# Optimization experiments

Hardware: AMD Instinct MI355X
Metric: run time of the kernel (lower is better)

## Reference

```python
import jax, jax.numpy as jnp
import numpy as np
import math

D_MODEL, D_STATE, D_CONV, EXPAND = 1024, 16, 4, 2
D_INNER = EXPAND * D_MODEL
DT_RANK = math.ceil(D_MODEL / 16)
BATCH, SEQLEN = 2, 2048


def setup_inputs() -> dict:
    key = jax.random.key(0)
    ks = jax.random.split(key, 10)
    hidden_states = jax.random.normal(ks[0], (BATCH, SEQLEN, D_MODEL), dtype=jnp.float32)
    in_proj_w = jax.random.normal(ks[1], (2 * D_INNER, D_MODEL), dtype=jnp.float32) / math.sqrt(D_MODEL)
    conv_w = jax.random.normal(ks[2], (D_INNER, 1, D_CONV), dtype=jnp.float32) / math.sqrt(D_CONV)
    conv_b = jnp.zeros((D_INNER,), dtype=jnp.float32)
    x_proj_w = jax.random.normal(ks[3], (DT_RANK + 2 * D_STATE, D_INNER), dtype=jnp.float32) / math.sqrt(D_INNER)
    dt_init_std = DT_RANK ** (-0.5)
    dt_proj_w = jax.random.uniform(ks[4], (D_INNER, DT_RANK), dtype=jnp.float32, minval=-dt_init_std, maxval=dt_init_std)
    # dt bias: inverse softplus of dt ~ LogUniform(1e-3, 1e-1), as in the original init
    dt = jnp.exp(jax.random.uniform(ks[5], (D_INNER,), dtype=jnp.float32) * (math.log(0.1) - math.log(0.001)) + math.log(0.001))
    dt = jnp.clip(dt, 1e-4, None)
    dt_proj_b = dt + jnp.log(-jnp.expm1(-dt))
    # A = -exp(A_log), A_log = log(1..d_state) broadcast over d_inner
    A_log = jnp.log(jnp.tile(jnp.arange(1, D_STATE + 1, dtype=jnp.float32)[None, :], (D_INNER, 1)))
    D = jnp.ones((D_INNER,), dtype=jnp.float32)
    out_proj_w = jax.random.normal(ks[6], (D_MODEL, D_INNER), dtype=jnp.float32) / math.sqrt(D_INNER)
    return {
        'hidden_states': hidden_states, 'in_proj_w': in_proj_w, 'conv_w': conv_w,
        'conv_b': conv_b, 'x_proj_w': x_proj_w, 'dt_proj_w': dt_proj_w,
        'dt_proj_b': dt_proj_b, 'A_log': A_log, 'D': D, 'out_proj_w': out_proj_w,
    }


def reference(hidden_states, in_proj_w, conv_w, conv_b, x_proj_w, dt_proj_w, dt_proj_b, A_log, D, out_proj_w):
    B_, L, _ = hidden_states.shape
    d_inner, d_state = A_log.shape
    K = conv_w.shape[-1]
    dt_rank = x_proj_w.shape[0] - 2 * d_state

    # in_proj: (b,l,d_model) -> (b,l,2*d_inner); split into x, z
    xz = hidden_states @ in_proj_w.T
    x, z = jnp.split(xz, 2, axis=-1)

    # causal depthwise conv1d (padding=K-1, truncated to seqlen) + SiLU
    w = conv_w[:, 0, :]  # (d_inner, K)
    xp = jnp.pad(x, ((0, 0), (K - 1, 0), (0, 0)))
    x = sum(xp[:, k:k + L, :] * w[:, k] for k in range(K)) + conv_b
    x = jax.nn.silu(x)

    # x_proj -> dt, B, C
    x_dbl = x @ x_proj_w.T  # (b,l,dt_rank+2n)
    dt, Bm, Cm = jnp.split(x_dbl, [dt_rank, dt_rank + d_state], axis=-1)
    delta = jax.nn.softplus(dt @ dt_proj_w.T + dt_proj_b)  # (b,l,d_inner)
    A = -jnp.exp(A_log)  # (d_inner, d_state)

    # selective scan over time
    def step(h, inp):
        d_t, B_t, C_t, u_t = inp  # (b,d),(b,n),(b,n),(b,d)
        dA = jnp.exp(d_t[:, :, None] * A)                      # (b,d,n)
        h = h * dA + (d_t * u_t)[:, :, None] * B_t[:, None, :]  # (b,d,n)
        y = jnp.einsum('bdn,bn->bd', h, C_t)
        return h, y

    h0 = jnp.zeros((B_, d_inner, d_state), dtype=hidden_states.dtype)
    xs = (jnp.swapaxes(delta, 0, 1), jnp.swapaxes(Bm, 0, 1),
          jnp.swapaxes(Cm, 0, 1), jnp.swapaxes(x, 0, 1))
    _, ys = jax.lax.scan(step, h0, xs)  # ys: (l,b,d_inner)
    y = jnp.swapaxes(ys, 0, 1) + D * x
    y = y * jax.nn.silu(z)
    return y @ out_proj_w.T  # (b,l,d_model)
```

## Files before the change

### kernel.cpp

```cpp
#include <hip/hip_runtime.h>
#include <hip/hip_bf16.h>
#include <math.h>
#include <stddef.h>

#define BATCH   2
#define SEQLEN  2048
#define DMODEL  1024
#define DINNER  2048
#define DSTATE  16
#define DCONV   4
#define DTRANK  64
#define NROWS   (BATCH*SEQLEN)
#define LCH     32
#define NCH     (SEQLEN/LCH)
#define MB      1048576

using ab_frag = __attribute__((ext_vector_type(8))) short;
using cd_frag = __attribute__((ext_vector_type(4))) float;

__device__ __forceinline__ unsigned short f2bf(float f) {
    unsigned u = __float_as_uint(f);
    u = (u + 0x7FFFu + ((u >> 16) & 1u)) >> 16;
    return (unsigned short)u;
}
__device__ __forceinline__ float bf2f(unsigned short h) {
    return __uint_as_float(((unsigned)h) << 16);
}

__device__ __forceinline__ void gll16(const unsigned short* g, unsigned short* l) {
    __builtin_amdgcn_global_load_lds(
        (const __attribute__((address_space(1))) void*)g,
        (__attribute__((address_space(3))) void*)l, 16, 0, 0);
}

__device__ __forceinline__ void pow_chain(float q, float* e) {
    float q2 = q * q;
    float q4 = q2 * q2;
    float q8 = q4 * q4;
    e[0] = q;       e[1] = q2;      e[2] = q2 * q;  e[3] = q4;
    e[4] = q4 * q;  e[5] = q4 * q2; e[6] = q4 * q2 * q; e[7] = q8;
    e[8] = q8 * q;  e[9] = q8 * q2; e[10] = q8 * q2 * q; e[11] = q8 * q4;
    e[12] = q8 * q4 * q; e[13] = q8 * q4 * q2; e[14] = q8 * q4 * q2 * q;
    e[15] = q8 * q8;
}

__global__ void cvt_multi(
    const float* __restrict__ s0, unsigned short* __restrict__ d0, int n0,
    const float* __restrict__ s1, unsigned short* __restrict__ d1, int n1,
    const float* __restrict__ s2, unsigned short* __restrict__ d2, int n2,
    const float* __restrict__ s3, unsigned short* __restrict__ d3, int n3,
    const float* __restrict__ s4, unsigned short* __restrict__ d4, int n4)
{
    int i = blockIdx.x * 256 + threadIdx.x;
    const float* s; unsigned short* d;
    if (i < n0)              { s = s0; d = d0; }
    else if ((i -= n0) < n1) { s = s1; d = d1; }
    else if ((i -= n1) < n2) { s = s2; d = d2; }
    else if ((i -= n2) < n3) { s = s3; d = d3; }
    else if ((i -= n3) < n4) { s = s4; d = d4; }
    else return;
    float4 v = ((const float4*)s)[i];
    ushort4 o;
    o.x = f2bf(v.x); o.y = f2bf(v.y); o.z = f2bf(v.z); o.w = f2bf(v.w);
    ((ushort4*)d)[i] = o;
}

__global__ void reduce2(const float* __restrict__ p, float* __restrict__ out, int n4) {
    int i = blockIdx.x * 256 + threadIdx.x;
    if (i < n4) {
        float4 a = ((const float4*)p)[i];
        float4 b = ((const float4*)p)[i + 1048576];
        float4 o; o.x = a.x + b.x; o.y = a.y + b.y; o.z = a.z + b.z; o.w = a.w + b.w;
        ((float4*)out)[i] = o;
    }
}

__global__ void reduce8_cvt(const float* __restrict__ p,
                            float* __restrict__ xdbl,
                            unsigned short* __restrict__ xdblbf, int n4) {
    int i = blockIdx.x * 256 + threadIdx.x;
    if (i < n4) {
        float4 a = ((const float4*)p)[i];
#pragma unroll
        for (int s = 1; s < 8; ++s) {
            float4 b = ((const float4*)p)[i + (size_t)s * n4];
            a.x += b.x; a.y += b.y; a.z += b.z; a.w += b.w;
        }
        ((float4*)xdbl)[i] = a;
        ushort4 o;
        o.x = f2bf(a.x); o.y = f2bf(a.y); o.z = f2bf(a.z); o.w = f2bf(a.w);
        ((ushort4*)xdblbf)[i] = o;
    }
}

__global__ __launch_bounds__(512, 2) void gemm1_8ph(
    const unsigned short* __restrict__ A,
    const unsigned short* __restrict__ W,
    unsigned short* __restrict__ X, unsigned short* __restrict__ Z)
{
    __shared__ unsigned short As[2][2][8192];
    __shared__ unsigned short Bs[2][2][8192];

    const int tid  = threadIdx.x;
    const int lane = tid & 63;
    const int wave = tid >> 6;
    const int l15  = lane & 15;
    const int quad = lane >> 4;
    const int wm   = wave >> 2;
    const int wn   = wave & 3;
    const int wbh  = wn >> 1;

    int bid = blockIdx.x;
    int wg  = (bid & 7) * 32 + (bid >> 3);
    const int by = wg >> 4;
    const int bx = wg & 15;
    const int mBase = by * 256;
    const int nBase = bx * 256;

    const int srow   = tid >> 3;
    const int schunk = (tid & 7) ^ (srow & 7);
    const unsigned short* gA = A + (size_t)(mBase + srow) * 1024 + schunk * 8;
    const unsigned short* gB = W + (size_t)(nBase + srow) * 1024 + schunk * 8;

#define STAGE_A(BB, H, T) do {                                          \
    const unsigned short* _s = gA + (size_t)(H) * 131072 + (T) * 64;    \
    gll16(_s,         &As[BB][H][wave * 512]);                          \
    gll16(_s + 65536, &As[BB][H][wave * 512 + 4096]);                   \
} while (0)
#define STAGE_B(BB, H, T) do {                                          \
    const unsigned short* _s = gB + (size_t)(H) * 131072 + (T) * 64;    \
    gll16(_s,         &Bs[BB][H][wave * 512]);                          \
    gll16(_s + 65536, &Bs[BB][H][wave * 512 + 4096]);                   \
} while (0)

    const int swz  = l15 & 7;
    const int cA0  = ((quad ^ swz) & 7) * 8;
    const int cA1  = (((4 + quad) ^ swz) & 7) * 8;
    const int aOff = l15 * 64;
    const int bOff = (wn & 1) * 4096 + l15 * 64;

#define LDA8(DST, BUF, HOFF)                                                     \
    _Pragma("unroll")                                                            \
    for (int rb = 0; rb < 4; ++rb) {                                             \
        DST[rb * 2 + 0] = *(const ab_frag*)(&As[BUF][wm][(HOFF) + rb * 1024 + aOff + cA0]); \
        DST[rb * 2 + 1] = *(const ab_frag*)(&As[BUF][wm][(HOFF) + rb * 1024 + aOff + cA1]); \
    }
#define LDB4(DST, BUF, CBOFF)                                                    \
    _Pragma("unroll")                                                            \
    for (int cb = 0; cb < 2; ++cb) {                                             \
        DST[cb * 2 + 0] = *(const ab_frag*)(&Bs[BUF][wbh][(CBOFF) + cb * 1024 + bOff + cA0]); \
        DST[cb * 2 + 1] = *(const ab_frag*)(&Bs[BUF][wbh][(CBOFF) + cb * 1024 + bOff + cA1]); \
    }
#define MMA16(R0, C0, AARR, BF)                                                  \
    __builtin_amdgcn_s_setprio(1);                                               \
    _Pragma("unroll")                                                            \
    for (int rb = 0; rb < 4; ++rb)                                               \
        _Pragma("unroll")                                                        \
        for (int cb = 0; cb < 2; ++cb) {                                         \
            acc[(R0) + rb][(C0) + cb] = __builtin_amdgcn_mfma_f32_16x16x32_bf16( \
                AARR[rb * 2 + 0], BF[cb * 2 + 0], acc[(R0) + rb][(C0) + cb], 0, 0, 0); \
            acc[(R0) + rb][(C0) + cb] = __builtin_amdgcn_mfma_f32_16x16x32_bf16( \
                AARR[rb * 2 + 1], BF[cb * 2 + 1], acc[(R0) + rb][(C0) + cb], 0, 0, 0); \
        }                                                                        \
    __builtin_amdgcn_s_setprio(0);

    cd_frag acc[8][4];
#pragma unroll
    for (int i = 0; i < 8; ++i)
#pragma unroll
        for (int j = 0; j < 4; ++j)
            acc[i][j] = (cd_frag){0.f, 0.f, 0.f, 0.f};

    ab_frag a0[8], a1[8], bA[4], bB[4];

    STAGE_A(0, 0, 0); STAGE_A(0, 1, 0);
    STAGE_B(0, 0, 0); STAGE_B(0, 1, 0);
    STAGE_B(1, 0, 1); STAGE_B(1, 1, 1);
    asm volatile("s_waitcnt vmcnt(4)" ::: "memory");
    __builtin_amdgcn_s_barrier();
    LDA8(a0, 0, 0);
    LDB4(bA, 0, 0);

    for (int t = 0; t < 16; ++t) {
        const int cur = t & 1, nb = cur ^ 1;
        LDB4(bB, cur, 2048);
        if (t + 1 < 16) STAGE_A(nb, 0, t + 1);
        asm volatile("s_waitcnt lgkmcnt(4)" ::: "memory");
        MMA16(0, 0, a0, bA);
        LDA8(a1, cur, 4096);
        if (t + 1 < 16) STAGE_A(nb, 1, t + 1);
        asm volatile("s_waitcnt lgkmcnt(8)" ::: "memory");
        MMA16(0, 2, a0, bB);
        __builtin_amdgcn_s_barrier();
        if (t + 2 < 16) { STAGE_B(cur, 0, t + 2); STAGE_B(cur, 1, t + 2); }
        asm volatile("s_waitcnt lgkmcnt(0)" ::: "memory");
        MMA16(4, 2, a1, bB);
        if (t < 15) {
            if (t < 14) { asm volatile("s_waitcnt vmcnt(4)" ::: "memory"); }
            else        { asm volatile("s_waitcnt vmcnt(0)" ::: "memory"); }
            __builtin_amdgcn_s_barrier();
            LDA8(a0, nb, 0);
            __builtin_amdgcn_sched_barrier(0);
            MMA16(4, 0, a1, bA);
            LDB4(bA, nb, 0);
        } else {
            MMA16(4, 0, a1, bA);
        }
    }

    unsigned short* OutP = (nBase < 2048) ? X : Z;
    const int colBase = (nBase < 2048) ? nBase : nBase - 2048;
#pragma unroll
    for (int rb = 0; rb < 8; ++rb)
#pragma unroll
        for (int cb = 0; cb < 4; ++cb) {
            int r0 = mBase + wm * 128 + rb * 16 + quad * 4;
            int cc = colBase + wn * 64 + cb * 16 + l15;
#pragma unroll
            for (int rg = 0; rg < 4; ++rg)
                OutP[(size_t)(r0 + rg) * 2048 + cc] = f2bf(acc[rb][cb][rg]);
        }
#undef STAGE_A
#undef STAGE_B
#undef LDA8
#undef LDB4
#undef MMA16
}

template<int EPI>
__global__ __launch_bounds__(256) void gemm_bf16_nt(
    const unsigned short* __restrict__ A, int lda,
    const unsigned short* __restrict__ W, int ldw,
    void* __restrict__ Cp, int ldc,
    int M, int N, int K,
    const float* __restrict__ bias)
{
    __shared__ unsigned short As[3][4096];
    __shared__ unsigned short Ws[3][4096];
    const int tid  = threadIdx.x;
    const int lane = tid & 63;
    const int wave = tid >> 6;
    const int l15  = lane & 15;
    const int quad = lane >> 4;
    const int wrow = (wave >> 1) * 64;
    const int wcol = (wave & 1) * 64;
    const int bx = blockIdx.x, by = blockIdx.y;
    const int mBase = by * 128;
    const int nBase = bx * 128;
    const int kStart = blockIdx.z * K;

    const int sRow = wave * 32 + (lane >> 2);
    const int sK   = (lane & 3) * 8;
    const unsigned short* gA = A + (size_t)(mBase + sRow) * lda + kStart + sK;
    const unsigned short* gB = W + (size_t)(nBase + sRow) * ldw + kStart + sK;
    const int woff = wave * 1024;

    cd_frag acc[4][4];
#pragma unroll
    for (int i = 0; i < 4; ++i)
#pragma unroll
        for (int j = 0; j < 4; ++j)
            acc[i][j] = (cd_frag){0.f, 0.f, 0.f, 0.f};

#pragma unroll
    for (int p = 0; p < 2; ++p) {
        gll16(gA, &As[p][woff]);
        gll16(gA + (size_t)16 * lda, &As[p][woff + 512]);
        gll16(gB, &Ws[p][woff]);
        gll16(gB + (size_t)16 * ldw, &Ws[p][woff + 512]);
        gA += 32; gB += 32;
    }

    const int nIter = K >> 5;
    int cb = 0;
    for (int it = 0; it < nIter; ++it) {
        if (it + 1 < nIter) {
            asm volatile("s_waitcnt vmcnt(4)" ::: "memory");
        } else {
            asm volatile("s_waitcnt vmcnt(0)" ::: "memory");
        }
        asm volatile("s_waitcnt lgkmcnt(0)" ::: "memory");
        __builtin_amdgcn_s_barrier();
        if (it + 2 < nIter) {
            int pb = cb >= 1 ? cb - 1 : cb + 2;
            gll16(gA, &As[pb][woff]);
            gll16(gA + (size_t)16 * lda, &As[pb][woff + 512]);
            gll16(gB, &Ws[pb][woff]);
            gll16(gB + (size_t)16 * ldw, &Ws[pb][woff + 512]);
            gA += 32; gB += 32;
        }
        ab_frag af[4], bfr[4];
#pragma unroll
        for (int i = 0; i < 4; ++i) {
            af[i]  = *(const ab_frag*)(&As[cb][(wrow + i * 16 + l15) * 32 + quad * 8]);
            bfr[i] = *(const ab_frag*)(&Ws[cb][(wcol + i * 16 + l15) * 32 + quad * 8]);
        }
#pragma unroll
        for (int mi = 0; mi < 4; ++mi)
#pragma unroll
            for (int ni = 0; ni < 4; ++ni) {
                acc[mi][ni] = __builtin_amdgcn_mfma_f32_16x16x32_bf16(
                    af[mi], bfr[ni], acc[mi][ni], 0, 0, 0);
            }
        cb = cb < 2 ? cb + 1 : 0;
    }

#pragma unroll
    for (int mi = 0; mi < 4; ++mi)
#pragma unroll
        for (int ni = 0; ni < 4; ++ni) {
            int r0 = mBase + wrow + mi * 16 + quad * 4;
            int cc = nBase + wcol + ni * 16 + l15;
            if (cc < N) {
#pragma unroll
                for (int rg = 0; rg < 4; ++rg) {
                    float v = acc[mi][ni][rg];
                    size_t r = (size_t)(r0 + rg);
                    if (EPI == 2) {
                        float x = v + bias[cc];
                        float e = __expf(-fabsf(x));
                        float sp = fmaxf(x, 0.f) + __logf(1.f + e);
                        ((unsigned short*)Cp)[r * ldc + cc] = f2bf(sp);
                    } else {
                        ((float*)Cp)[(size_t)blockIdx.z * M * ldc + r * ldc + cc] = v;
                    }
                }
            }
        }
}

__global__ void conv_silu_kernel(const unsigned short* __restrict__ xb,
                                 const float* __restrict__ cw,
                                 const float* __restrict__ cb,
                                 unsigned short* __restrict__ xcbf) {
    int i  = blockIdx.x * 256 + threadIdx.x;
    int d  = i & (DINNER - 1);
    int lq = (i >> 11) & 511;
    int b  = i >> 20;
    int l0 = lq * 4;
    const unsigned short* base = xb + (size_t)b * SEQLEN * DINNER + d;
    float w0 = cw[d * 4], w1 = cw[d * 4 + 1], w2 = cw[d * 4 + 2], w3 = cw[d * 4 + 3];
    float x[7];
#pragma unroll
    for (int j = 0; j < 7; ++j) {
        int l = l0 - 3 + j;
        x[j] = (l >= 0) ? bf2f(base[(size_t)l * DINNER]) : 0.f;
    }
    float bias = cb[d];
    unsigned short* o = xcbf + (size_t)b * SEQLEN * DINNER + d;
#pragma unroll
    for (int j = 0; j < 4; ++j) {
        float s = bias + x[j] * w0 + x[j + 1] * w1 + x[j + 2] * w2 + x[j + 3] * w3;
        o[(size_t)(l0 + j) * DINNER] = f2bf(s / (1.f + __expf(-s)));
    }
}

__global__ __launch_bounds__(256) void scan_phase1(
    const unsigned short* __restrict__ delta, const unsigned short* __restrict__ xc,
    const float* __restrict__ xdbl,
    float* __restrict__ S, float* __restrict__ dsb)
{
    int d  = blockIdx.x * 256 + threadIdx.x;
    int ch = blockIdx.y;
    int b  = blockIdx.z;
    float h[16];
#pragma unroll
    for (int n = 0; n < 16; ++n) h[n] = 0.f;
    float dsum = 0.f;
    int t0 = ch * LCH;
    const unsigned short* dl = delta + ((size_t)b * SEQLEN + t0) * DINNER + d;
    const unsigned short* uc = xc + ((size_t)b * SEQLEN + t0) * DINNER + d;
    const float* bc = xdbl  + ((size_t)b * SEQLEN + t0) * 96 + 64;
    for (int t = 0; t < LCH; ++t) {
        float dv = bf2f(dl[(size_t)t * DINNER]);
        float u  = bf2f(uc[(size_t)t * DINNER]);
        const float4* bp = (const float4*)(bc + (size_t)t * 96);
        float4 B0 = bp[0], B1 = bp[1], B2 = bp[2], B3 = bp[3];
        float Bv[16] = {B0.x,B0.y,B0.z,B0.w, B1.x,B1.y,B1.z,B1.w,
                        B2.x,B2.y,B2.z,B2.w, B3.x,B3.y,B3.z,B3.w};
        float du = dv * u;
        dsum += dv;
        float e[16];
        pow_chain(__expf(-dv), e);
#pragma unroll
        for (int n = 0; n < 16; ++n)
            h[n] = h[n] * e[n] + du * Bv[n];
    }
    size_t base = ((size_t)(b * NCH + ch) * 16) << 11;
#pragma unroll
    for (int n = 0; n < 16; ++n)
        S[base + ((size_t)n << 11) + d] = h[n];
    dsb[(((size_t)(b * NCH + ch)) << 11) + d] = dsum;
}

__global__ void scan_phase2(const float* __restrict__ S,
                            const float* __restrict__ dsb,
                            const float* __restrict__ A_log,
                            float* __restrict__ H) {
    int i = blockIdx.x * 256 + threadIdx.x;
    int b = i >> 15;
    int n = (i >> 11) & 15;
    int d = i & 2047;
    float Adn = -__expf(A_log[d * 16 + n]);
    float h = 0.f;
    for (int c = 0; c < NCH; ++c) {
        size_t sidx = (((size_t)((b * NCH + c) * 16 + n)) << 11) + d;
        H[sidx] = h;
        float P = __expf(dsb[(((size_t)(b * NCH + c)) << 11) + d] * Adn);
        h = S[sidx] + P * h;
    }
}

__global__ __launch_bounds__(256) void scan_phase3(
    const unsigned short* __restrict__ delta, const unsigned short* __restrict__ xc,
    const float* __restrict__ xdbl,
    const float* __restrict__ Dv, const float* __restrict__ H,
    const unsigned short* __restrict__ zb, unsigned short* __restrict__ yg)
{
    int d  = blockIdx.x * 256 + threadIdx.x;
    int ch = blockIdx.y;
    int b  = blockIdx.z;
    float Dd = Dv[d];
    size_t hbase = ((size_t)(b * NCH + ch) * 16) << 11;
    float h[16];
#pragma unroll
    for (int n = 0; n < 16; ++n) h[n] = H[hbase + ((size_t)n << 11) + d];
    int t0 = ch * LCH;
    const unsigned short* dl = delta + ((size_t)b * SEQLEN + t0) * DINNER + d;
    const unsigned short* uc = xc + ((size_t)b * SEQLEN + t0) * DINNER + d;
    const unsigned short* zl = zb + ((size_t)b * SEQLEN + t0) * DINNER + d;
    const float* bc = xdbl  + ((size_t)b * SEQLEN + t0) * 96 + 64;
    unsigned short* yo = yg + ((size_t)b * SEQLEN + t0) * DINNER + d;
    for (int t = 0; t < LCH; ++t) {
        float dv = bf2f(dl[(size_t)t * DINNER]);
        float u  = bf2f(uc[(size_t)t * DINNER]);
        const float4* bp = (const float4*)(bc + (size_t)t * 96);
        float4 B0 = bp[0], B1 = bp[1], B2 = bp[2], B3 = bp[3];
        float4 C0 = bp[4], C1 = bp[5], C2 = bp[6], C3 = bp[7];
        float Bv[16] = {B0.x,B0.y,B0.z,B0.w, B1.x,B1.y,B1.z,B1.w,
                        B2.x,B2.y,B2.z,B2.w, B3.x,B3.y,B3.z,B3.w};
        float Cv[16] = {C0.x,C0.y,C0.z,C0.w, C1.x,C1.y,C1.z,C1.w,
                        C2.x,C2.y,C2.z,C2.w, C3.x,C3.y,C3.z,C3.w};
        float du = dv * u;
        float e[16];
        pow_chain(__expf(-dv), e);
#pragma unroll
        for (int n = 0; n < 16; ++n)
            h[n] = h[n] * e[n] + du * Bv[n];
        float y0 = 0.f, y1 = 0.f, y2 = 0.f, y3 = 0.f;
#pragma unroll
        for (int n = 0; n < 16; n += 4) {
            y0 += h[n+0] * Cv[n+0];
            y1 += h[n+1] * Cv[n+1];
            y2 += h[n+2] * Cv[n+2];
            y3 += h[n+3] * Cv[n+3];
        }
        float y = (y0 + y1) + (y2 + y3) + Dd * u;
        float z = bf2f(zl[(size_t)t * DINNER]);
        float g = z / (1.f + __expf(-z));
        yo[(size_t)t * DINNER] = f2bf(y * g);
    }
}

extern "C" void kernel_launch(void* const* d_in, const int* in_sizes, int n_in,
                              void* d_out, int out_size, void* d_ws, size_t ws_size,
                              hipStream_t stream) {
    const float* hidden    = (const float*)d_in[0];
    const float* in_proj_w = (const float*)d_in[1];
    const float* conv_w    = (const float*)d_in[2];
    const float* conv_b    = (const float*)d_in[3];
    const float* x_proj_w  = (const float*)d_in[4];
    const float* dt_proj_w = (const float*)d_in[5];
    const float* dt_proj_b = (const float*)d_in[6];
    const float* A_log     = (const float*)d_in[7];
    const float* Dvec      = (const float*)d_in[8];
    const float* out_proj_w= (const float*)d_in[9];
    float* out = (float*)d_out;

    char* ws = (char*)d_ws;
    unsigned short* xbf    = (unsigned short*)(ws + 0);
    float* Sbuf            = (float*)(ws + 0);
    unsigned short* zbf    = (unsigned short*)(ws + 16*MB);
    float* dsumbuf         = (float*)(ws + 32*MB);
    float* Hbuf            = (float*)(ws + 34*MB);
    unsigned short* deltabf= (unsigned short*)(ws + 50*MB);
    unsigned short* xcbf   = (unsigned short*)(ws + 66*MB);
    float* xdbl            = (float*)(ws + 82*MB);
    unsigned short* xdblbf = (unsigned short*)(ws + 84*MB);
    unsigned short* hbf    = (unsigned short*)(ws + 85*MB);
    unsigned short* w1bf   = (unsigned short*)(ws + 93*MB);
    float* xdbl_part       = (float*)(ws + 85*MB);
    unsigned short* xpwbf  = (unsigned short*)(ws + 101*MB);
    unsigned short* dtwbf  = (unsigned short*)(ws + 102*MB);
    unsigned short* outwbf = (unsigned short*)(ws + 103*MB);
    unsigned short* ygbf   = (unsigned short*)(ws + 107*MB);
    float* part            = (float*)(ws + 123*MB);

    cvt_multi<<<dim3(10560), 256, 0, stream>>>(
        hidden,     hbf,    1048576,
        in_proj_w,  w1bf,   1048576,
        out_proj_w, outwbf, 524288,
        x_proj_w,   xpwbf,  49152,
        dt_proj_w,  dtwbf,  32768);

    gemm1_8ph<<<dim3(256), 512, 0, stream>>>(hbf, w1bf, xbf, zbf);

    conv_silu_kernel<<<8192, 256, 0, stream>>>(xbf, conv_w, conv_b, xcbf);

    gemm_bf16_nt<4><<<dim3(1, 32, 8), 256, 0, stream>>>(
        xcbf, 2048, xpwbf, 2048, xdbl_part, 96, 4096, 96, 256, nullptr);

    reduce8_cvt<<<dim3(384), 256, 0, stream>>>(xdbl_part, xdbl, xdblbf, 98304);

    gemm_bf16_nt<2><<<dim3(16, 32), 256, 0, stream>>>(
        xdblbf, 96, dtwbf, 64, deltabf, 2048, 4096, 2048, 64, dt_proj_b);

    scan_phase1<<<dim3(8, NCH, BATCH), 256, 0, stream>>>(deltabf, xcbf, xdbl,
                                                         Sbuf, dsumbuf);
    scan_phase2<<<dim3(256), 256, 0, stream>>>(Sbuf, dsumbuf, A_log, Hbuf);
    scan_phase3<<<dim3(8, NCH, BATCH), 256, 0, stream>>>(deltabf, xcbf, xdbl,
                                                         Dvec, Hbuf, zbf, ygbf);

    gemm_bf16_nt<4><<<dim3(8, 32, 2), 256, 0, stream>>>(
        ygbf, 2048, outwbf, 2048, part, 1024, 4096, 1024, 1024, nullptr);
    reduce2<<<dim3(4096), 256, 0, stream>>>(part, out, 1048576);
}
```

Baseline: 267.9 us.

## Run out_proj on the pipelined 256x256 MFMA GEMM with 4-way split-K

Generalizes the in_proj 8-wave double-buffered GEMM into a template over leading dimension, K-tile count and epilogue. The out_proj GEMM now uses it with a 4-way K split, writing fp32 partials and summing them in a new reduce4 kernel. This replaces the smaller generic bf16 GEMM, but partial-sum traffic roughly doubles, from 2 to 4 slices. Separately, scan_phase2 is manually unrolled by 4 so that loads across chunks are issued together.

```diff
diff --git a/kernel.cpp b/kernel.cpp
--- a/kernel.cpp
+++ b/kernel.cpp
@@ -65,13 +65,16 @@
     ((ushort4*)d)[i] = o;
 }
 
-__global__ void reduce2(const float* __restrict__ p, float* __restrict__ out, int n4) {
+__global__ void reduce4(const float* __restrict__ p, float* __restrict__ out, int n4) {
     int i = blockIdx.x * 256 + threadIdx.x;
     if (i < n4) {
         float4 a = ((const float4*)p)[i];
-        float4 b = ((const float4*)p)[i + 1048576];
-        float4 o; o.x = a.x + b.x; o.y = a.y + b.y; o.z = a.z + b.z; o.w = a.w + b.w;
-        ((float4*)out)[i] = o;
+#pragma unroll
+        for (int s = 1; s < 4; ++s) {
+            float4 b = ((const float4*)p)[i + (size_t)s * 1048576];
+            a.x += b.x; a.y += b.y; a.z += b.z; a.w += b.w;
+        }
+        ((float4*)out)[i] = a;
     }
 }
 
@@ -93,10 +96,12 @@
     }
 }
 
-__global__ __launch_bounds__(512, 2) void gemm1_8ph(
+template<int LD, int NTILES, int EPI>
+__global__ __launch_bounds__(512, 2) void gemm_pipe(
     const unsigned short* __restrict__ A,
     const unsigned short* __restrict__ W,
-    unsigned short* __restrict__ X, unsigned short* __restrict__ Z)
+    unsigned short* __restrict__ X, unsigned short* __restrict__ Z,
+    float* __restrict__ P)
 {
     __shared__ unsigned short As[2][2][8192];
     __shared__ unsigned short Bs[2][2][8192];
@@ -111,26 +116,35 @@
     const int wbh  = wn >> 1;
 
     int bid = blockIdx.x;
-    int wg  = (bid & 7) * 32 + (bid >> 3);
-    const int by = wg >> 4;
-    const int bx = wg & 15;
-    const int mBase = by * 256;
-    const int nBase = bx * 256;
+    int by, bx, ksl;
+    if (EPI == 0) {
+        int wg = (bid & 7) * 32 + (bid >> 3);
+        by = wg >> 4; bx = wg & 15; ksl = 0;
+    } else {
+        int xcd = bid & 7, j = bid >> 3;
+        int p = xcd + 8 * (j >> 2);
+        bx  = j & 3;
+        by  = p >> 2;
+        ksl = p & 3;
+    }
+    const int mBase  = by * 256;
+    const int nBase  = bx * 256;
+    const int kStart = ksl * NTILES * 64;
 
     const int srow   = tid >> 3;
     const int schunk = (tid & 7) ^ (srow & 7);
-    const unsigned short* gA = A + (size_t)(mBase + srow) * 1024 + schunk * 8;
-    const unsigned short* gB = W + (size_t)(nBase + srow) * 1024 + schunk * 8;
-
-#define STAGE_A(BB, H, T) do {                                          \
-    const unsigned short* _s = gA + (size_t)(H) * 131072 + (T) * 64;    \
-    gll16(_s,         &As[BB][H][wave * 512]);                          \
-    gll16(_s + 65536, &As[BB][H][wave * 512 + 4096]);                   \
+    const unsigned short* gA = A + (size_t)(mBase + srow) * LD + kStart + schunk * 8;
+    const unsigned short* gB = W + (size_t)(nBase + srow) * LD + kStart + schunk * 8;
+
+#define STAGE_A(BB, H, T) do {                                            \
+    const unsigned short* _s = gA + (size_t)(H) * 128 * LD + (T) * 64;    \
+    gll16(_s,           &As[BB][H][wave * 512]);                          \
+    gll16(_s + 64 * LD, &As[BB][H][wave * 512 + 4096]);                   \
 } while (0)
-#define STAGE_B(BB, H, T) do {                                          \
-    const unsigned short* _s = gB + (size_t)(H) * 131072 + (T) * 64;    \
-    gll16(_s,         &Bs[BB][H][wave * 512]);                          \
-    gll16(_s + 65536, &Bs[BB][H][wave * 512 + 4096]);                   \
+#define STAGE_B(BB, H, T) do {                                            \
+    const unsigned short* _s = gB + (size_t)(H) * 128 * LD + (T) * 64;    \
+    gll16(_s,           &Bs[BB][H][wave * 512]);                          \
+    gll16(_s + 64 * LD, &Bs[BB][H][wave * 512 + 4096]);                   \
 } while (0)
 
     const int swz  = l15 & 7;
@@ -181,23 +195,23 @@
     LDA8(a0, 0, 0);
     LDB4(bA, 0, 0);
 
-    for (int t = 0; t < 16; ++t) {
+    for (int t = 0; t < NTILES; ++t) {
         const int cur = t & 1, nb = cur ^ 1;
         LDB4(bB, cur, 2048);
-        if (t + 1 < 16) STAGE_A(nb, 0, t + 1);
+        if (t + 1 < NTILES) STAGE_A(nb, 0, t + 1);
         asm volatile("s_waitcnt lgkmcnt(4)" ::: "memory");
         MMA16(0, 0, a0, bA);
         LDA8(a1, cur, 4096);
-        if (t + 1 < 16) STAGE_A(nb, 1, t + 1);
+        if (t + 1 < NTILES) STAGE_A(nb, 1, t + 1);
         asm volatile("s_waitcnt lgkmcnt(8)" ::: "memory");
         MMA16(0, 2, a0, bB);
         __builtin_amdgcn_s_barrier();
-        if (t + 2 < 16) { STAGE_B(cur, 0, t + 2); STAGE_B(cur, 1, t + 2); }
+        if (t + 2 < NTILES) { STAGE_B(cur, 0, t + 2); STAGE_B(cur, 1, t + 2); }
         asm volatile("s_waitcnt lgkmcnt(0)" ::: "memory");
         MMA16(4, 2, a1, bB);
-        if (t < 15) {
-            if (t < 14) { asm volatile("s_waitcnt vmcnt(4)" ::: "memory"); }
-            else        { asm volatile("s_waitcnt vmcnt(0)" ::: "memory"); }
+        if (t < NTILES - 1) {
+            if (t < NTILES - 2) { asm volatile("s_waitcnt vmcnt(4)" ::: "memory"); }
+            else                { asm volatile("s_waitcnt vmcnt(0)" ::: "memory"); }
             __builtin_amdgcn_s_barrier();
             LDA8(a0, nb, 0);
             __builtin_amdgcn_sched_barrier(0);
@@ -208,18 +222,32 @@
         }
     }
 
-    unsigned short* OutP = (nBase < 2048) ? X : Z;
-    const int colBase = (nBase < 2048) ? nBase : nBase - 2048;
-#pragma unroll
-    for (int rb = 0; rb < 8; ++rb)
-#pragma unroll
-        for (int cb = 0; cb < 4; ++cb) {
-            int r0 = mBase + wm * 128 + rb * 16 + quad * 4;
-            int cc = colBase + wn * 64 + cb * 16 + l15;
-#pragma unroll
-            for (int rg = 0; rg < 4; ++rg)
-                OutP[(size_t)(r0 + rg) * 2048 + cc] = f2bf(acc[rb][cb][rg]);
-        }
+    if (EPI == 0) {
+        unsigned short* OutP = (nBase < 2048) ? X : Z;
+        const int colBase = (nBase < 2048) ? nBase : nBase - 2048;
+#pragma unroll
+        for (int rb = 0; rb < 8; ++rb)
+#pragma unroll
+            for (int cb = 0; cb < 4; ++cb) {
+                int r0 = mBase + wm * 128 + rb * 16 + quad * 4;
+                int cc = colBase + wn * 64 + cb * 16 + l15;
+#pragma unroll
+                for (int rg = 0; rg < 4; ++rg)
+                    OutP[(size_t)(r0 + rg) * 2048 + cc] = f2bf(acc[rb][cb][rg]);
+            }
+    } else {
+        float* Pp = P + (size_t)ksl * 4194304;
+#pragma unroll
+        for (int rb = 0; rb < 8; ++rb)
+#pragma unroll
+            for (int cb = 0; cb < 4; ++cb) {
+                int r0 = mBase + wm * 128 + rb * 16 + quad * 4;
+                int cc = nBase + wn * 64 + cb * 16 + l15;
+#pragma unroll
+                for (int rg = 0; rg < 4; ++rg)
+                    Pp[(size_t)(r0 + rg) * 1024 + cc] = acc[rb][cb][rg];
+            }
+    }
 #undef STAGE_A
 #undef STAGE_B
 #undef LDA8
@@ -403,11 +431,17 @@
     int d = i & 2047;
     float Adn = -__expf(A_log[d * 16 + n]);
     float h = 0.f;
-    for (int c = 0; c < NCH; ++c) {
-        size_t sidx = (((size_t)((b * NCH + c) * 16 + n)) << 11) + d;
-        H[sidx] = h;
-        float P = __expf(dsb[(((size_t)(b * NCH + c)) << 11) + d] * Adn);
-        h = S[sidx] + P * h;
+    const float* Sp = S   + ((((size_t)(b * NCH) * 16 + n)) << 11) + d;
+    const float* Dp = dsb + (((size_t)(b * NCH)) << 11) + d;
+    float*       Hp = H   + ((((size_t)(b * NCH) * 16 + n)) << 11) + d;
+    for (int c = 0; c < NCH; c += 4) {
+        float s0 = Sp[0], s1 = Sp[32768], s2 = Sp[65536], s3 = Sp[98304];
+        float p0 = Dp[0], p1 = Dp[2048],  p2 = Dp[4096],  p3 = Dp[6144];
+        Hp[0]     = h;  h = s0 + __expf(p0 * Adn) * h;
+        Hp[32768] = h;  h = s1 + __expf(p1 * Adn) * h;
+        Hp[65536] = h;  h = s2 + __expf(p2 * Adn) * h;
+        Hp[98304] = h;  h = s3 + __expf(p3 * Adn) * h;
+        Sp += 131072; Dp += 8192; Hp += 131072;
     }
 }
 
@@ -503,7 +537,7 @@
         x_proj_w,   xpwbf,  49152,
         dt_proj_w,  dtwbf,  32768);
 
-    gemm1_8ph<<<dim3(256), 512, 0, stream>>>(hbf, w1bf, xbf, zbf);
+    gemm_pipe<1024, 16, 0><<<dim3(256), 512, 0, stream>>>(hbf, w1bf, xbf, zbf, nullptr);
 
     conv_silu_kernel<<<8192, 256, 0, stream>>>(xbf, conv_w, conv_b, xcbf);
 
@@ -521,7 +555,7 @@
     scan_phase3<<<dim3(8, NCH, BATCH), 256, 0, stream>>>(deltabf, xcbf, xdbl,
                                                          Dvec, Hbuf, zbf, ygbf);
 
-    gemm_bf16_nt<4><<<dim3(8, 32, 2), 256, 0, stream>>>(
-        ygbf, 2048, outwbf, 2048, part, 1024, 4096, 1024, 1024, nullptr);
-    reduce2<<<dim3(4096), 256, 0, stream>>>(part, out, 1048576);
-}
+    gemm_pipe<2048, 8, 1><<<dim3(256), 512, 0, stream>>>(
+        ygbf, outwbf, nullptr, nullptr, part);
+    reduce4<<<dim3(4096), 256, 0, stream>>>(part, out, 1048576);
+}
```

Result: no change. 272.7 us (+1.8%).
